# Kernel tuning notes

Hardware: AMD Instinct MI355X
Metric: run time of the kernel (lower is better)

## Reference

```python
import jax, jax.numpy as jnp
import numpy as np


def setup_inputs() -> dict:
    key = jax.random.key(0)
    k1, k2, k3 = jax.random.split(key, 3)
    N, F, E, H = 50000, 256, 800000, 4
    P = F // H + 1            # proj = 65
    dk = P * H                # 260
    x = jax.random.normal(k1, (N, F), dtype=jnp.float32)
    W = jax.random.normal(k2, (2 * dk, F), dtype=jnp.float32) * 0.02
    b = jnp.zeros((2 * dk,), dtype=jnp.float32)
    edge_index = jax.random.randint(k3, (2, E), 0, N, dtype=jnp.int32)
    return {"x": x, "edge_index": edge_index, "W": W, "b": b, "num_heads": H}


def reference(x, edge_index, W, b, num_heads):
    # x: [N, F]; W: [2*dk, F] with dk = P*num_heads; edge_index: [2, E]
    N = x.shape[0]
    P = W.shape[0] // (2 * num_heads)
    qk = x @ W.T + b                                   # [N, 2*dk]
    qk = qk.reshape(N, num_heads, 2 * P)               # 'L (h hdim) -> L h hdim'
    q, k = qk[..., :P], qk[..., P:]                    # split=2 outer -> q then k, each [N, H, P]
    src, dst = edge_index[0], edge_index[1]
    # per-edge dot product per head (NB: original never applies self.scale)
    scores = jnp.einsum('ehp,ehp->eh', q[src], k[dst])  # [E, H]
    # sparse softmax over dim=2 (columns) i.e. segment-softmax grouped by row index per head
    smax = jax.ops.segment_max(scores, src, num_segments=N)  # [N, H]
    ex = jnp.exp(scores - smax[src])                         # [E, H]
    denom = jax.ops.segment_sum(ex, src, num_segments=N)     # [N, H]
    attn = ex / denom[src]                                   # [E, H]
    # torch.sparse.sum(attn, dim=0) / num_heads -> mean over heads per edge
    vals = attn.mean(axis=1)                                 # [E]
    return vals
```

## Files before the change

### kernel.cpp

```cpp
#include <hip/hip_runtime.h>
#include <hip/hip_bf16.h>

#define K_DIM 256
#define RQ    512
#define NPAD  640
#define GBM 128
#define GBN 128
#define GBK 32
#define EPITCH 152
#define NBK   104
#define CBLK  256
#define SBAND 12512
#define DBAND 25024

typedef unsigned short u16;
using short8  = __attribute__((ext_vector_type(8))) short;
using ushort8 = __attribute__((ext_vector_type(8))) unsigned short;
using f32x4   = __attribute__((ext_vector_type(4))) float;
using f32x2   = __attribute__((ext_vector_type(2))) float;

__device__ __forceinline__ float asf(unsigned u) {
  union { unsigned i; float f; } x; x.i = u; return x.f;
}
__device__ __forceinline__ u16 f2b(float f) {
  __hip_bfloat16 h = __float2bfloat16(f); return *(u16*)&h;
}

__device__ __forceinline__ int bucket_of(int s, int d) {
  int sband = s / SBAND;
  int dband = d / DBAND;
  int ssub  = (s - sband * SBAND) >> 10;
  return ((sband << 1) | dband) * 13 + ssub;
}

__device__ __forceinline__ int map2(int p) {
  if (p < 256) return (p >> 6) * 130 + (p & 63);
  if (p < 512) { int q = p - 256; return (q >> 6) * 130 + 65 + (q & 63); }
  if (p < 516) return (p - 512) * 130 + 64;
  if (p < 520) return (p - 516) * 130 + 129;
  return -1;
}

__global__ void __launch_bounds__(256) prep(
    const float* __restrict__ x, const float* __restrict__ W,
    const float* __restrict__ bv, const int* __restrict__ ei,
    u16* __restrict__ xb, u16* __restrict__ wb,
    float* __restrict__ bias, float* __restrict__ zbase,
    int* __restrict__ counts,
    int M, int Mpad, int E, int per, int xblocks, int wblocks, int zblocks)
{
  __shared__ int h[NBK];
  const int blk = blockIdx.x, tid = threadIdx.x;
  if (blk < xblocks) {
    int idx = blk * 256 + tid;
    int total = Mpad * (K_DIM / 8);
    if (idx >= total) return;
    int row = idx / (K_DIM / 8);
    ushort8 o;
    if (row < M) {
      const float* s = x + (size_t)idx * 8;
      float4 a = *(const float4*)s;
      float4 b = *(const float4*)(s + 4);
      o[0] = f2b(a.x); o[1] = f2b(a.y); o[2] = f2b(a.z); o[3] = f2b(a.w);
      o[4] = f2b(b.x); o[5] = f2b(b.y); o[6] = f2b(b.z); o[7] = f2b(b.w);
    } else {
      #pragma unroll
      for (int j = 0; j < 8; ++j) o[j] = 0;
    }
    *(ushort8*)(xb + (size_t)idx * 8) = o;
  } else if (blk < xblocks + wblocks) {
    int idx = (blk - xblocks) * 256 + tid;
    int total = NPAD * (K_DIM / 8);
    if (idx >= total) return;
    int p  = idx / (K_DIM / 8);
    int kc = (idx % (K_DIM / 8)) * 8;
    int c  = map2(p);
    ushort8 o;
    if (c >= 0) {
      const float* s = W + (size_t)c * K_DIM + kc;
      float4 a = *(const float4*)s;
      float4 v = *(const float4*)(s + 4);
      o[0] = f2b(a.x); o[1] = f2b(a.y); o[2] = f2b(a.z); o[3] = f2b(a.w);
      o[4] = f2b(v.x); o[5] = f2b(v.y); o[6] = f2b(v.z); o[7] = f2b(v.w);
    } else {
      #pragma unroll
      for (int j = 0; j < 8; ++j) o[j] = 0;
    }
    *(ushort8*)(wb + (size_t)idx * 8) = o;
    if (kc == 0) bias[p] = (c >= 0) ? bv[c] : 0.f;
  } else if (blk < xblocks + wblocks + zblocks) {
    int i = (blk - xblocks - wblocks) * 256 + tid;
    if (i < M * 4) zbase[i] = 0.f;
  } else {
    int cb = blk - xblocks - wblocks - zblocks;
    if (tid < NBK) h[tid] = 0;
    __syncthreads();
    int start = cb * per, end = min(start + per, E);
    for (int i = start + tid; i < end; i += 256)
      atomicAdd(&h[bucket_of(ei[i], ei[E + i])], 1);
    __syncthreads();
    if (tid < NBK) counts[tid * CBLK + cb] = h[tid];
  }
}

__global__ void __launch_bounds__(256) gemm_mfma(
    const u16* __restrict__ xb, const u16* __restrict__ wb,
    const float* __restrict__ bias, u16* __restrict__ qkb,
    u16* __restrict__ tl, int M)
{
  __shared__ u16 smem[GBM * EPITCH];
  const int tid  = threadIdx.x;
  const int wave = tid >> 6, lane = tid & 63;
  const int l15 = lane & 15, lhi = lane >> 4;
  const int row0 = blockIdx.x * GBM, p0 = blockIdx.y * GBN;
  const int wr = (wave >> 1) * 64, wc = (wave & 1) * 64;

  f32x4 acc[4][4];
  #pragma unroll
  for (int m = 0; m < 4; ++m)
    #pragma unroll
    for (int n = 0; n < 4; ++n) acc[m][n] = (f32x4){0.f, 0.f, 0.f, 0.f};

#define STAGE(b, k0) do {                                                     \
    u16* As_ = smem + (b) * 8192;                                             \
    u16* Bs_ = As_ + 4096;                                                    \
    _Pragma("unroll")                                                         \
    for (int i_ = 0; i_ < 2; ++i_) {                                          \
      int f_ = wave * 128 + i_ * 64 + lane;                                   \
      int r_ = f_ >> 2, c_ = f_ & 3;                                          \
      const u16* gA = xb + (size_t)(row0 + r_) * K_DIM + (k0) + c_ * 8;       \
      __builtin_amdgcn_global_load_lds(                                       \
          (const __attribute__((address_space(1))) void*)gA,                  \
          (__attribute__((address_space(3))) void*)(As_ + (wave*128 + i_*64)*8), \
          16, 0, 0);                                                          \
      const u16* gB = wb + (size_t)(p0 + r_) * K_DIM + (k0) + c_ * 8;         \
      __builtin_amdgcn_global_load_lds(                                       \
          (const __attribute__((address_space(1))) void*)gB,                  \
          (__attribute__((address_space(3))) void*)(Bs_ + (wave*128 + i_*64)*8), \
          16, 0, 0);                                                          \
    }                                                                         \
  } while (0)

  STAGE(0, 0);
  asm volatile("s_waitcnt vmcnt(0)" ::: "memory");
  __syncthreads();

  #pragma unroll
  for (int t = 0; t < K_DIM / GBK; ++t) {
    if (t < K_DIM / GBK - 1) STAGE((t + 1) & 1, (t + 1) * GBK);
    const u16* As = smem + (t & 1) * 8192;
    const u16* Bs = As + 4096;
    short8 af[4], bf[4];
    #pragma unroll
    for (int m = 0; m < 4; ++m)
      af[m] = *(const short8*)(As + (size_t)(wr + m * 16 + l15) * GBK + lhi * 8);
    #pragma unroll
    for (int n = 0; n < 4; ++n)
      bf[n] = *(const short8*)(Bs + (size_t)(wc + n * 16 + l15) * GBK + lhi * 8);
    #pragma unroll
    for (int m = 0; m < 4; ++m)
      #pragma unroll
      for (int n = 0; n < 4; ++n)
        acc[m][n] = __builtin_amdgcn_mfma_f32_16x16x32_bf16(af[m], bf[n], acc[m][n], 0, 0, 0);
    if (t < K_DIM / GBK - 1) {
      asm volatile("s_waitcnt vmcnt(0)" ::: "memory");
      __syncthreads();
    }
  }
#undef STAGE

  __syncthreads();

  #pragma unroll
  for (int n = 0; n < 4; ++n) {
    int col = wc + n * 16 + l15;
    float bvv = bias[p0 + col];
    #pragma unroll
    for (int m = 0; m < 4; ++m) {
      #pragma unroll
      for (int r = 0; r < 4; ++r) {
        int row = wr + m * 16 + lhi * 4 + r;
        smem[row * EPITCH + col] = f2b(acc[m][n][r] + bvv);
      }
    }
  }
  __syncthreads();

  if (p0 < 512) {
    #pragma unroll
    for (int it = 0; it < 8; ++it) {
      int row  = wave * 32 + it * 4 + lhi;
      int grow = row0 + row;
      uint4 v = *(const uint4*)(smem + row * EPITCH + l15 * 8);
      if (grow < M)
        *(uint4*)(qkb + (size_t)grow * RQ + p0 + l15 * 8) = v;
    }
  } else {
    #pragma unroll
    for (int it = 0; it < 8; ++it) {
      int row  = wave * 32 + it * 4 + lhi;
      int grow = row0 + row;
      if (l15 == 0 && grow < M) {
        uint4 v = *(const uint4*)(smem + row * EPITCH);
        *(uint4*)(tl + (size_t)grow * 8) = v;
      }
    }
  }
}

__global__ void __launch_bounds__(1024) scan_k(int* __restrict__ counts)
{
  __shared__ int tot[NBK], base[NBK];
  const int tid = threadIdx.x, wv = tid >> 6, ln = tid & 63;
  for (int k = wv; k < NBK; k += 16) {
    int sum = 0;
    #pragma unroll
    for (int c = 0; c < CBLK / 64; ++c) sum += counts[k * CBLK + c * 64 + ln];
    #pragma unroll
    for (int off = 1; off < 64; off <<= 1) sum += __shfl_xor(sum, off);
    if (ln == 0) tot[k] = sum;
  }
  __syncthreads();
  if (tid == 0) {
    int run = 0;
    for (int k = 0; k < NBK; ++k) { base[k] = run; run += tot[k]; }
  }
  __syncthreads();
  for (int k = wv; k < NBK; k += 16) {
    int carry = base[k];
    #pragma unroll
    for (int c = 0; c < CBLK / 64; ++c) {
      int v = counts[k * CBLK + c * 64 + ln];
      int inc = v;
      #pragma unroll
      for (int off = 1; off < 64; off <<= 1) {
        int u = __shfl_up(inc, off);
        if (ln >= off) inc += u;
      }
      int last = __shfl(inc, 63);
      counts[k * CBLK + c * 64 + ln] = carry + inc - v;
      carry += last;
    }
  }
}

__global__ void __launch_bounds__(256) scatter2_k(
    const int* __restrict__ ei, const int* __restrict__ offs,
    uint2* __restrict__ sorted, int E, int per)
{
  __shared__ int cur[NBK];
  const int tid = threadIdx.x, blk = blockIdx.x;
  if (tid < NBK) cur[tid] = offs[tid * CBLK + blk];
  __syncthreads();
  int start = blk * per, end = min(start + per, E);
  for (int i = start + tid; i < end; i += 256) {
    int s = ei[i], d = ei[E + i];
    int pos = atomicAdd(&cur[bucket_of(s, d)], 1);
    sorted[pos] = make_uint2(((unsigned)s << 16) | (unsigned)d, (unsigned)i);
  }
}

__global__ void __launch_bounds__(256) edge_pass(
    const u16* __restrict__ qkb, const u16* __restrict__ tl,
    const uint2* __restrict__ sorted,
    float* __restrict__ exb, float* __restrict__ denom, int E)
{
  const int tid  = threadIdx.x;
  const int wave = tid >> 6, lane = tid & 63;
  const int g = lane >> 3;
  const int l = lane & 7;

  const int nwg = gridDim.x;
  const int q8 = nwg >> 3, r8 = nwg & 7;
  const int xcd = blockIdx.x & 7, bix = blockIdx.x >> 3;
  const int swz = (xcd < r8) ? (xcd * (q8 + 1) + bix)
                             : (r8 * (q8 + 1) + (xcd - r8) * q8 + bix);

  const int slot = swz * 32 + wave * 8 + g;
  const bool valid = slot < E;
  uint2 tr = sorted[valid ? slot : 0];
  const int src = tr.x >> 16, dst = tr.x & 0xffff;
  const int e = tr.y;

  const u16* qrow = qkb + ((size_t)src * RQ) + l * 32;
  const u16* krow = qkb + ((size_t)dst * RQ) + 256 + l * 32;

  int2 ti = make_int2(0, 0);
  if (l < 2) {
    const u16* tp = tl + (size_t)(l ? dst : src) * 8 + (l ? 4 : 0);
    ti = *(const int2*)tp;
  }

  f32x2 a2 = {0.f, 0.f};
  #pragma unroll
  for (int c = 0; c < 4; ++c) {
    uint4 qv = *(const uint4*)(qrow + c * 8);
    uint4 kv = *(const uint4*)(krow + c * 8);
    const unsigned* qd = (const unsigned*)&qv;
    const unsigned* kd = (const unsigned*)&kv;
    #pragma unroll
    for (int j = 0; j < 4; ++j) {
      f32x2 qa = { asf(qd[j] << 16), asf(qd[j] & 0xffff0000u) };
      f32x2 ka = { asf(kd[j] << 16), asf(kd[j] & 0xffff0000u) };
      a2 += qa * ka;
    }
  }
  float s = a2[0] + a2[1];
  s += __shfl_xor(s, 1);

  const int h = l >> 1;
  int idxA = ((g << 3) | (l & 1)) << 2;
  int w01 = __builtin_amdgcn_ds_bpermute(idxA, ti.x);
  int w23 = __builtin_amdgcn_ds_bpermute(idxA, ti.y);
  unsigned wsel = (h & 2) ? (unsigned)w23 : (unsigned)w01;
  float tv = (h & 1) ? asf(wsel & 0xffff0000u) : asf(wsel << 16);
  float to = __shfl_xor(tv, 1);
  s = fmaf(tv, to, s);

  float ev = __expf(s);
  if (valid && (l & 1) == 0) {
    exb[(size_t)e * 4 + h] = ev;
    unsafeAtomicAdd(&denom[(size_t)src * 4 + h], ev);
  }
}

__global__ void __launch_bounds__(256) finalize_k(
    const float* __restrict__ exb, const float* __restrict__ denom,
    const int* __restrict__ ei, float* __restrict__ out, int E)
{
  int e = blockIdx.x * 256 + threadIdx.x;
  if (e >= E) return;
  int src = ei[e];
  float4 ev = *(const float4*)(exb + (size_t)e * 4);
  float4 dv = *(const float4*)(denom + (size_t)src * 4);
  out[e] = 0.25f * (ev.x / dv.x + ev.y / dv.y + ev.z / dv.z + ev.w / dv.w);
}

extern "C" void kernel_launch(void* const* d_in, const int* in_sizes, int n_in,
                              void* d_out, int out_size, void* d_ws, size_t ws_size,
                              hipStream_t stream)
{
  const float* x  = (const float*)d_in[0];
  const int*   ei = (const int*)d_in[1];
  const float* W  = (const float*)d_in[2];
  const float* b  = (const float*)d_in[3];

  const int F = in_sizes[2] / in_sizes[3];
  const int M = in_sizes[0] / F;
  const int E = in_sizes[1] / 2;

  const int mblocks = (M + GBM - 1) / GBM;
  const int Mpad    = mblocks * GBM;

  u16* xb  = (u16*)d_ws;
  u16* wb  = xb + (size_t)Mpad * K_DIM;
  u16* qkb = wb + (size_t)NPAD * K_DIM;
  u16* tl  = qkb + (size_t)M * RQ;
  float* bias  = (float*)(tl + (size_t)M * 8);
  float* exb   = bias + NPAD;
  float* denom = exb + (size_t)E * 4;
  int*   counts = (int*)(denom + (size_t)M * 4);
  uint2* sorted = (uint2*)(counts + NBK * CBLK);

  const int xblocks = (Mpad * (K_DIM / 8) + 255) / 256;
  const int wblocks = (NPAD * (K_DIM / 8) + 255) / 256;
  const int zblocks = (M * 4 + 255) / 256;
  const int per     = (E + CBLK - 1) / CBLK;
  hipLaunchKernelGGL(prep, dim3(xblocks + wblocks + zblocks + CBLK), dim3(256), 0,
                     stream, x, W, b, ei, xb, wb, bias, denom, counts,
                     M, Mpad, E, per, xblocks, wblocks, zblocks);

  hipLaunchKernelGGL(scan_k, dim3(1), dim3(1024), 0, stream, counts);

  dim3 gg(mblocks, NPAD / GBN);
  hipLaunchKernelGGL(gemm_mfma, gg, dim3(256), 0, stream, xb, wb, bias, qkb, tl, M);

  hipLaunchKernelGGL(scatter2_k, dim3(CBLK), dim3(256), 0, stream,
                     ei, counts, sorted, E, per);

  int eblocks = (E + 31) / 32;
  hipLaunchKernelGGL(edge_pass, dim3(eblocks), dim3(256), 0, stream,
                     qkb, tl, sorted, exb, denom, E);

  hipLaunchKernelGGL(finalize_k, dim3((E + 255) / 256), dim3(256), 0, stream,
                     exb, denom, ei, (float*)d_out, E);
}
```

Measured before the change: 176.8 us.

## Fuse x bf16 conversion into GEMM, keep A tile resident, store exp in fp16

```diff
diff --git a/kernel.cpp b/kernel.cpp
--- a/kernel.cpp
+++ b/kernel.cpp
@@ -5,9 +5,6 @@
 #define RQ    512
 #define NPAD  640
 #define GBM 128
-#define GBN 128
-#define GBK 32
-#define EPITCH 152
 #define NBK   104
 #define CBLK  256
 #define SBAND 12512
@@ -25,6 +22,8 @@
 __device__ __forceinline__ u16 f2b(float f) {
   __hip_bfloat16 h = __float2bfloat16(f); return *(u16*)&h;
 }
+__device__ __forceinline__ u16 f2h(float f) { _Float16 h = (_Float16)f; return *(u16*)&h; }
+__device__ __forceinline__ float h2f(u16 u) { _Float16 h = *(_Float16*)&u; return (float)h; }
 
 __device__ __forceinline__ int bucket_of(int s, int d) {
   int sband = s / SBAND;
@@ -42,34 +41,16 @@
 }
 
 __global__ void __launch_bounds__(256) prep(
-    const float* __restrict__ x, const float* __restrict__ W,
-    const float* __restrict__ bv, const int* __restrict__ ei,
-    u16* __restrict__ xb, u16* __restrict__ wb,
-    float* __restrict__ bias, float* __restrict__ zbase,
+    const float* __restrict__ W, const float* __restrict__ bv,
+    const int* __restrict__ ei,
+    u16* __restrict__ wb, float* __restrict__ bias, float* __restrict__ zbase,
     int* __restrict__ counts,
-    int M, int Mpad, int E, int per, int xblocks, int wblocks, int zblocks)
+    int M, int E, int per, int wblocks, int zblocks)
 {
   __shared__ int h[NBK];
   const int blk = blockIdx.x, tid = threadIdx.x;
-  if (blk < xblocks) {
+  if (blk < wblocks) {
     int idx = blk * 256 + tid;
-    int total = Mpad * (K_DIM / 8);
-    if (idx >= total) return;
-    int row = idx / (K_DIM / 8);
-    ushort8 o;
-    if (row < M) {
-      const float* s = x + (size_t)idx * 8;
-      float4 a = *(const float4*)s;
-      float4 b = *(const float4*)(s + 4);
-      o[0] = f2b(a.x); o[1] = f2b(a.y); o[2] = f2b(a.z); o[3] = f2b(a.w);
-      o[4] = f2b(b.x); o[5] = f2b(b.y); o[6] = f2b(b.z); o[7] = f2b(b.w);
-    } else {
-      #pragma unroll
-      for (int j = 0; j < 8; ++j) o[j] = 0;
-    }
-    *(ushort8*)(xb + (size_t)idx * 8) = o;
-  } else if (blk < xblocks + wblocks) {
-    int idx = (blk - xblocks) * 256 + tid;
     int total = NPAD * (K_DIM / 8);
     if (idx >= total) return;
     int p  = idx / (K_DIM / 8);
@@ -88,11 +69,11 @@
     }
     *(ushort8*)(wb + (size_t)idx * 8) = o;
     if (kc == 0) bias[p] = (c >= 0) ? bv[c] : 0.f;
-  } else if (blk < xblocks + wblocks + zblocks) {
-    int i = (blk - xblocks - wblocks) * 256 + tid;
+  } else if (blk < wblocks + zblocks) {
+    int i = (blk - wblocks) * 256 + tid;
     if (i < M * 4) zbase[i] = 0.f;
   } else {
-    int cb = blk - xblocks - wblocks - zblocks;
+    int cb = blk - wblocks - zblocks;
     if (tid < NBK) h[tid] = 0;
     __syncthreads();
     int start = cb * per, end = min(start + per, E);
@@ -103,17 +84,55 @@
   }
 }
 
-__global__ void __launch_bounds__(256) gemm_mfma(
-    const u16* __restrict__ xb, const u16* __restrict__ wb,
+__global__ void __launch_bounds__(256) gemm_fused(
+    const float* __restrict__ x, const u16* __restrict__ wb,
     const float* __restrict__ bias, u16* __restrict__ qkb,
     u16* __restrict__ tl, int M)
 {
-  __shared__ u16 smem[GBM * EPITCH];
+  __shared__ u16 A[GBM * K_DIM];
+  __shared__ u16 Bb[2 * 512 * 8];
   const int tid  = threadIdx.x;
   const int wave = tid >> 6, lane = tid & 63;
   const int l15 = lane & 15, lhi = lane >> 4;
-  const int row0 = blockIdx.x * GBM, p0 = blockIdx.y * GBN;
+  const int row0 = blockIdx.x * GBM;
   const int wr = (wave >> 1) * 64, wc = (wave & 1) * 64;
+  const int sw = l15 & 7;
+
+  #pragma unroll
+  for (int it = 0; it < 16; ++it) {
+    int f  = it * 256 + tid;
+    int r  = f >> 5, ch = f & 31;
+    int grow = row0 + r;
+    float4 a0 = make_float4(0.f,0.f,0.f,0.f), a1 = a0;
+    if (grow < M) {
+      const float* s = x + (size_t)grow * K_DIM + ch * 8;
+      a0 = *(const float4*)s;
+      a1 = *(const float4*)(s + 4);
+    }
+    ushort8 o;
+    o[0] = f2b(a0.x); o[1] = f2b(a0.y); o[2] = f2b(a0.z); o[3] = f2b(a0.w);
+    o[4] = f2b(a1.x); o[5] = f2b(a1.y); o[6] = f2b(a1.z); o[7] = f2b(a1.w);
+    *(ushort8*)(A + r * K_DIM + (ch ^ (r & 7)) * 8) = o;
+  }
+
+#define BLOAD(i, va, vb) do {                                                  \
+    int p_ = (i) >> 3, kt_ = (i) & 7;                                          \
+    const u16* base_ = wb + (size_t)(p_ * 128) * K_DIM + kt_ * 32;             \
+    int r1_ = tid >> 2, c1_ = tid & 3;                                         \
+    va = *(const uint4*)(base_ + (size_t)r1_ * K_DIM + c1_ * 8);               \
+    int r2_ = (tid + 256) >> 2, c2_ = tid & 3;                                 \
+    vb = *(const uint4*)(base_ + (size_t)r2_ * K_DIM + c2_ * 8);               \
+  } while (0)
+#define BWRITE(i, va, vb) do {                                                 \
+    u16* bb_ = Bb + ((i) & 1) * 4096;                                          \
+    int r1_ = tid >> 2, c1_ = tid & 3;                                         \
+    *(uint4*)(bb_ + (c1_ * 128 + r1_) * 8) = va;                               \
+    int r2_ = (tid + 256) >> 2, c2_ = tid & 3;                                 \
+    *(uint4*)(bb_ + (c2_ * 128 + r2_) * 8) = vb;                               \
+  } while (0)
+
+  { uint4 b0a, b0b; BLOAD(0, b0a, b0b); BWRITE(0, b0a, b0b); }
+  __syncthreads();
 
   f32x4 acc[4][4];
   #pragma unroll
@@ -121,91 +140,53 @@
     #pragma unroll
     for (int n = 0; n < 4; ++n) acc[m][n] = (f32x4){0.f, 0.f, 0.f, 0.f};
 
-#define STAGE(b, k0) do {                                                     \
-    u16* As_ = smem + (b) * 8192;                                             \
-    u16* Bs_ = As_ + 4096;                                                    \
-    _Pragma("unroll")                                                         \
-    for (int i_ = 0; i_ < 2; ++i_) {                                          \
-      int f_ = wave * 128 + i_ * 64 + lane;                                   \
-      int r_ = f_ >> 2, c_ = f_ & 3;                                          \
-      const u16* gA = xb + (size_t)(row0 + r_) * K_DIM + (k0) + c_ * 8;       \
-      __builtin_amdgcn_global_load_lds(                                       \
-          (const __attribute__((address_space(1))) void*)gA,                  \
-          (__attribute__((address_space(3))) void*)(As_ + (wave*128 + i_*64)*8), \
-          16, 0, 0);                                                          \
-      const u16* gB = wb + (size_t)(p0 + r_) * K_DIM + (k0) + c_ * 8;         \
-      __builtin_amdgcn_global_load_lds(                                       \
-          (const __attribute__((address_space(1))) void*)gB,                  \
-          (__attribute__((address_space(3))) void*)(Bs_ + (wave*128 + i_*64)*8), \
-          16, 0, 0);                                                          \
-    }                                                                         \
-  } while (0)
-
-  STAGE(0, 0);
-  asm volatile("s_waitcnt vmcnt(0)" ::: "memory");
-  __syncthreads();
-
-  #pragma unroll
-  for (int t = 0; t < K_DIM / GBK; ++t) {
-    if (t < K_DIM / GBK - 1) STAGE((t + 1) & 1, (t + 1) * GBK);
-    const u16* As = smem + (t & 1) * 8192;
-    const u16* Bs = As + 4096;
+  for (int i = 0; i < 40; ++i) {
+    const int kt = i & 7, buf = i & 1;
+    uint4 na, nb;
+    if (i < 39) BLOAD(i + 1, na, nb);
+
+    const u16* bbuf = Bb + buf * 4096;
     short8 af[4], bf[4];
+    const int cc = ((kt * 4 + lhi) ^ sw);
     #pragma unroll
     for (int m = 0; m < 4; ++m)
-      af[m] = *(const short8*)(As + (size_t)(wr + m * 16 + l15) * GBK + lhi * 8);
+      af[m] = *(const short8*)(A + (wr + m * 16 + l15) * K_DIM + cc * 8);
     #pragma unroll
     for (int n = 0; n < 4; ++n)
-      bf[n] = *(const short8*)(Bs + (size_t)(wc + n * 16 + l15) * GBK + lhi * 8);
+      bf[n] = *(const short8*)(bbuf + (lhi * 128 + wc + n * 16 + l15) * 8);
     #pragma unroll
     for (int m = 0; m < 4; ++m)
       #pragma unroll
       for (int n = 0; n < 4; ++n)
         acc[m][n] = __builtin_amdgcn_mfma_f32_16x16x32_bf16(af[m], bf[n], acc[m][n], 0, 0, 0);
-    if (t < K_DIM / GBK - 1) {
-      asm volatile("s_waitcnt vmcnt(0)" ::: "memory");
-      __syncthreads();
-    }
-  }
-#undef STAGE
-
-  __syncthreads();
-
-  #pragma unroll
-  for (int n = 0; n < 4; ++n) {
-    int col = wc + n * 16 + l15;
-    float bvv = bias[p0 + col];
-    #pragma unroll
-    for (int m = 0; m < 4; ++m) {
+
+    if (i < 39) BWRITE(i + 1, na, nb);
+    __syncthreads();
+
+    if (kt == 7) {
+      const int p0 = (i >> 3) * 128;
       #pragma unroll
-      for (int r = 0; r < 4; ++r) {
-        int row = wr + m * 16 + lhi * 4 + r;
-        smem[row * EPITCH + col] = f2b(acc[m][n][r] + bvv);
+      for (int n = 0; n < 4; ++n) {
+        int col = p0 + wc + n * 16 + l15;
+        float bvv = bias[col];
+        #pragma unroll
+        for (int m = 0; m < 4; ++m) {
+          #pragma unroll
+          for (int r = 0; r < 4; ++r) {
+            int grow = row0 + wr + m * 16 + lhi * 4 + r;
+            if (grow < M) {
+              float v = acc[m][n][r] + bvv;
+              if (col < 512)            qkb[(size_t)grow * RQ + col] = f2b(v);
+              else if (col < 520)       tl[(size_t)grow * 8 + col - 512] = f2b(v);
+            }
+          }
+          acc[m][n] = (f32x4){0.f, 0.f, 0.f, 0.f};
+        }
       }
     }
   }
-  __syncthreads();
-
-  if (p0 < 512) {
-    #pragma unroll
-    for (int it = 0; it < 8; ++it) {
-      int row  = wave * 32 + it * 4 + lhi;
-      int grow = row0 + row;
-      uint4 v = *(const uint4*)(smem + row * EPITCH + l15 * 8);
-      if (grow < M)
-        *(uint4*)(qkb + (size_t)grow * RQ + p0 + l15 * 8) = v;
-    }
-  } else {
-    #pragma unroll
-    for (int it = 0; it < 8; ++it) {
-      int row  = wave * 32 + it * 4 + lhi;
-      int grow = row0 + row;
-      if (l15 == 0 && grow < M) {
-        uint4 v = *(const uint4*)(smem + row * EPITCH);
-        *(uint4*)(tl + (size_t)grow * 8) = v;
-      }
-    }
-  }
+#undef BLOAD
+#undef BWRITE
 }
 
 __global__ void __launch_bounds__(1024) scan_k(int* __restrict__ counts)
@@ -263,7 +244,7 @@
 __global__ void __launch_bounds__(256) edge_pass(
     const u16* __restrict__ qkb, const u16* __restrict__ tl,
     const uint2* __restrict__ sorted,
-    float* __restrict__ exb, float* __restrict__ denom, int E)
+    u16* __restrict__ exh, float* __restrict__ denom, int E)
 {
   const int tid  = threadIdx.x;
   const int wave = tid >> 6, lane = tid & 63;
@@ -319,21 +300,22 @@
 
   float ev = __expf(s);
   if (valid && (l & 1) == 0) {
-    exb[(size_t)e * 4 + h] = ev;
+    exh[(size_t)e * 4 + h] = f2h(ev);
     unsafeAtomicAdd(&denom[(size_t)src * 4 + h], ev);
   }
 }
 
 __global__ void __launch_bounds__(256) finalize_k(
-    const float* __restrict__ exb, const float* __restrict__ denom,
+    const u16* __restrict__ exh, const float* __restrict__ denom,
     const int* __restrict__ ei, float* __restrict__ out, int E)
 {
   int e = blockIdx.x * 256 + threadIdx.x;
   if (e >= E) return;
   int src = ei[e];
-  float4 ev = *(const float4*)(exb + (size_t)e * 4);
+  ushort4 ev = *(const ushort4*)(exh + (size_t)e * 4);
   float4 dv = *(const float4*)(denom + (size_t)src * 4);
-  out[e] = 0.25f * (ev.x / dv.x + ev.y / dv.y + ev.z / dv.z + ev.w / dv.w);
+  out[e] = 0.25f * (h2f(ev.x) / dv.x + h2f(ev.y) / dv.y
+                  + h2f(ev.z) / dv.z + h2f(ev.w) / dv.w);
 }
 
 extern "C" void kernel_launch(void* const* d_in, const int* in_sizes, int n_in,
@@ -350,38 +332,35 @@
   const int E = in_sizes[1] / 2;
 
   const int mblocks = (M + GBM - 1) / GBM;
-  const int Mpad    = mblocks * GBM;
-
-  u16* xb  = (u16*)d_ws;
-  u16* wb  = xb + (size_t)Mpad * K_DIM;
+
+  u16* wb  = (u16*)d_ws;
   u16* qkb = wb + (size_t)NPAD * K_DIM;
   u16* tl  = qkb + (size_t)M * RQ;
   float* bias  = (float*)(tl + (size_t)M * 8);
-  float* exb   = bias + NPAD;
-  float* denom = exb + (size_t)E * 4;
+  u16*   exh   = (u16*)(bias + NPAD);
+  float* denom = (float*)(exh + (size_t)E * 4);
   int*   counts = (int*)(denom + (size_t)M * 4);
   uint2* sorted = (uint2*)(counts + NBK * CBLK);
 
-  const int xblocks = (Mpad * (K_DIM / 8) + 255) / 256;
   const int wblocks = (NPAD * (K_DIM / 8) + 255) / 256;
   const int zblocks = (M * 4 + 255) / 256;
   const int per     = (E + CBLK - 1) / CBLK;
-  hipLaunchKernelGGL(prep, dim3(xblocks + wblocks + zblocks + CBLK), dim3(256), 0,
-                     stream, x, W, b, ei, xb, wb, bias, denom, counts,
-                     M, Mpad, E, per, xblocks, wblocks, zblocks);
+  hipLaunchKernelGGL(prep, dim3(wblocks + zblocks + CBLK), dim3(256), 0, stream,
+                     W, b, ei, wb, bias, denom, counts,
+                     M, E, per, wblocks, zblocks);
 
   hipLaunchKernelGGL(scan_k, dim3(1), dim3(1024), 0, stream, counts);
 
-  dim3 gg(mblocks, NPAD / GBN);
-  hipLaunchKernelGGL(gemm_mfma, gg, dim3(256), 0, stream, xb, wb, bias, qkb, tl, M);
+  hipLaunchKernelGGL(gemm_fused, dim3(mblocks), dim3(256), 0, stream,
+                     x, wb, bias, qkb, tl, M);
 
   hipLaunchKernelGGL(scatter2_k, dim3(CBLK), dim3(256), 0, stream,
                      ei, counts, sorted, E, per);
 
   int eblocks = (E + 31) / 32;
   hipLaunchKernelGGL(edge_pass, dim3(eblocks), dim3(256), 0, stream,
-                     qkb, tl, sorted, exb, denom, E);
+                     qkb, tl, sorted, exh, denom, E);
 
   hipLaunchKernelGGL(finalize_k, dim3((E + 255) / 256), dim3(256), 0, stream,
-                     exb, denom, ei, (float*)d_out, E);
-}
+                     exh, denom, ei, (float*)d_out, E);
+}
```

Result: slower. 209.5 us (+18.5%).

## Split tail columns into separate GEMV and store edge exponentials as fp16

Applied to the files above, without the earlier changes.

```diff
diff --git a/kernel.cpp b/kernel.cpp
--- a/kernel.cpp
+++ b/kernel.cpp
@@ -3,7 +3,7 @@
 
 #define K_DIM 256
 #define RQ    512
-#define NPAD  640
+#define NW    512
 #define GBM 128
 #define GBN 128
 #define GBK 32
@@ -25,6 +25,11 @@
 __device__ __forceinline__ u16 f2b(float f) {
   __hip_bfloat16 h = __float2bfloat16(f); return *(u16*)&h;
 }
+__device__ __forceinline__ float b2f(u16 u) {
+  union { unsigned i; float f; } x; x.i = ((unsigned)u) << 16; return x.f;
+}
+__device__ __forceinline__ u16 f2h(float f) { _Float16 h = (_Float16)f; return *(u16*)&h; }
+__device__ __forceinline__ float h2f(u16 u) { _Float16 h = *(_Float16*)&u; return (float)h; }
 
 __device__ __forceinline__ int bucket_of(int s, int d) {
   int sband = s / SBAND;
@@ -35,10 +40,10 @@
 
 __device__ __forceinline__ int map2(int p) {
   if (p < 256) return (p >> 6) * 130 + (p & 63);
-  if (p < 512) { int q = p - 256; return (q >> 6) * 130 + 65 + (q & 63); }
-  if (p < 516) return (p - 512) * 130 + 64;
-  if (p < 520) return (p - 516) * 130 + 129;
-  return -1;
+  int q = p - 256; return (q >> 6) * 130 + 65 + (q & 63);
+}
+__device__ __forceinline__ int wrow_tail(int c) {
+  return (c < 4) ? c * 130 + 64 : (c - 4) * 130 + 129;
 }
 
 __global__ void __launch_bounds__(256) prep(
@@ -70,24 +75,19 @@
     *(ushort8*)(xb + (size_t)idx * 8) = o;
   } else if (blk < xblocks + wblocks) {
     int idx = (blk - xblocks) * 256 + tid;
-    int total = NPAD * (K_DIM / 8);
+    int total = NW * (K_DIM / 8);
     if (idx >= total) return;
     int p  = idx / (K_DIM / 8);
     int kc = (idx % (K_DIM / 8)) * 8;
     int c  = map2(p);
+    const float* s = W + (size_t)c * K_DIM + kc;
+    float4 a = *(const float4*)s;
+    float4 v = *(const float4*)(s + 4);
     ushort8 o;
-    if (c >= 0) {
-      const float* s = W + (size_t)c * K_DIM + kc;
-      float4 a = *(const float4*)s;
-      float4 v = *(const float4*)(s + 4);
-      o[0] = f2b(a.x); o[1] = f2b(a.y); o[2] = f2b(a.z); o[3] = f2b(a.w);
-      o[4] = f2b(v.x); o[5] = f2b(v.y); o[6] = f2b(v.z); o[7] = f2b(v.w);
-    } else {
-      #pragma unroll
-      for (int j = 0; j < 8; ++j) o[j] = 0;
-    }
+    o[0] = f2b(a.x); o[1] = f2b(a.y); o[2] = f2b(a.z); o[3] = f2b(a.w);
+    o[4] = f2b(v.x); o[5] = f2b(v.y); o[6] = f2b(v.z); o[7] = f2b(v.w);
     *(ushort8*)(wb + (size_t)idx * 8) = o;
-    if (kc == 0) bias[p] = (c >= 0) ? bv[c] : 0.f;
+    if (kc == 0) bias[p] = bv[c];
   } else if (blk < xblocks + wblocks + zblocks) {
     int i = (blk - xblocks - wblocks) * 256 + tid;
     if (i < M * 4) zbase[i] = 0.f;
@@ -105,8 +105,7 @@
 
 __global__ void __launch_bounds__(256) gemm_mfma(
     const u16* __restrict__ xb, const u16* __restrict__ wb,
-    const float* __restrict__ bias, u16* __restrict__ qkb,
-    u16* __restrict__ tl, int M)
+    const float* __restrict__ bias, u16* __restrict__ qkb, int M)
 {
   __shared__ u16 smem[GBM * EPITCH];
   const int tid  = threadIdx.x;
@@ -186,25 +185,60 @@
   }
   __syncthreads();
 
-  if (p0 < 512) {
-    #pragma unroll
-    for (int it = 0; it < 8; ++it) {
-      int row  = wave * 32 + it * 4 + lhi;
-      int grow = row0 + row;
-      uint4 v = *(const uint4*)(smem + row * EPITCH + l15 * 8);
-      if (grow < M)
-        *(uint4*)(qkb + (size_t)grow * RQ + p0 + l15 * 8) = v;
-    }
-  } else {
-    #pragma unroll
-    for (int it = 0; it < 8; ++it) {
-      int row  = wave * 32 + it * 4 + lhi;
-      int grow = row0 + row;
-      if (l15 == 0 && grow < M) {
-        uint4 v = *(const uint4*)(smem + row * EPITCH);
-        *(uint4*)(tl + (size_t)grow * 8) = v;
-      }
-    }
+  #pragma unroll
+  for (int it = 0; it < 8; ++it) {
+    int row  = wave * 32 + it * 4 + lhi;
+    int grow = row0 + row;
+    uint4 v = *(const uint4*)(smem + row * EPITCH + l15 * 8);
+    if (grow < M)
+      *(uint4*)(qkb + (size_t)grow * RQ + p0 + l15 * 8) = v;
+  }
+}
+
+__global__ void __launch_bounds__(256) tail_gemv(
+    const float* __restrict__ x, const float* __restrict__ W,
+    const float* __restrict__ bv, u16* __restrict__ tl, int M)
+{
+  __shared__ u16 wt[8 * 256];
+  __shared__ float tb[8];
+  const int tid = threadIdx.x;
+  #pragma unroll
+  for (int c = 0; c < 8; ++c)
+    wt[c * 256 + tid] = f2b(W[(size_t)wrow_tail(c) * K_DIM + tid]);
+  if (tid < 8) tb[tid] = bv[wrow_tail(tid)];
+  __syncthreads();
+
+  const int wave = tid >> 6, lane = tid & 63;
+  const int seg = lane & 7;
+  const int grow = blockIdx.x * 32 + wave * 8 + (lane >> 3);
+  const bool vr = grow < M;
+  const float* xr = x + (size_t)(vr ? grow : 0) * K_DIM + seg * 32;
+
+  float acc[8];
+  #pragma unroll
+  for (int c = 0; c < 8; ++c) acc[c] = 0.f;
+  #pragma unroll
+  for (int j = 0; j < 8; ++j) {
+    float4 xv = vr ? *(const float4*)(xr + j * 4) : make_float4(0.f,0.f,0.f,0.f);
+    #pragma unroll
+    for (int c = 0; c < 8; ++c) {
+      ushort4 wv = *(const ushort4*)(wt + c * 256 + seg * 32 + j * 4);
+      acc[c] = fmaf(xv.x, b2f(wv.x), acc[c]);
+      acc[c] = fmaf(xv.y, b2f(wv.y), acc[c]);
+      acc[c] = fmaf(xv.z, b2f(wv.z), acc[c]);
+      acc[c] = fmaf(xv.w, b2f(wv.w), acc[c]);
+    }
+  }
+  #pragma unroll
+  for (int off = 1; off < 8; off <<= 1)
+    #pragma unroll
+    for (int c = 0; c < 8; ++c) acc[c] += __shfl_xor(acc[c], off);
+
+  if (vr && seg == 0) {
+    ushort8 o;
+    #pragma unroll
+    for (int c = 0; c < 8; ++c) o[c] = f2b(acc[c] + tb[c]);
+    *(ushort8*)(tl + (size_t)grow * 8) = o;
   }
 }
 
@@ -263,7 +297,7 @@
 __global__ void __launch_bounds__(256) edge_pass(
     const u16* __restrict__ qkb, const u16* __restrict__ tl,
     const uint2* __restrict__ sorted,
-    float* __restrict__ exb, float* __restrict__ denom, int E)
+    u16* __restrict__ exh, float* __restrict__ denom, int E)
 {
   const int tid  = threadIdx.x;
   const int wave = tid >> 6, lane = tid & 63;
@@ -319,21 +353,22 @@
 
   float ev = __expf(s);
   if (valid && (l & 1) == 0) {
-    exb[(size_t)e * 4 + h] = ev;
+    exh[(size_t)e * 4 + h] = f2h(ev);
     unsafeAtomicAdd(&denom[(size_t)src * 4 + h], ev);
   }
 }
 
 __global__ void __launch_bounds__(256) finalize_k(
-    const float* __restrict__ exb, const float* __restrict__ denom,
+    const u16* __restrict__ exh, const float* __restrict__ denom,
     const int* __restrict__ ei, float* __restrict__ out, int E)
 {
   int e = blockIdx.x * 256 + threadIdx.x;
   if (e >= E) return;
   int src = ei[e];
-  float4 ev = *(const float4*)(exb + (size_t)e * 4);
+  ushort4 ev = *(const ushort4*)(exh + (size_t)e * 4);
   float4 dv = *(const float4*)(denom + (size_t)src * 4);
-  out[e] = 0.25f * (ev.x / dv.x + ev.y / dv.y + ev.z / dv.z + ev.w / dv.w);
+  out[e] = 0.25f * (h2f(ev.x) / dv.x + h2f(ev.y) / dv.y
+                  + h2f(ev.z) / dv.z + h2f(ev.w) / dv.w);
 }
 
 extern "C" void kernel_launch(void* const* d_in, const int* in_sizes, int n_in,
@@ -354,16 +389,16 @@
 
   u16* xb  = (u16*)d_ws;
   u16* wb  = xb + (size_t)Mpad * K_DIM;
-  u16* qkb = wb + (size_t)NPAD * K_DIM;
+  u16* qkb = wb + (size_t)NW * K_DIM;
   u16* tl  = qkb + (size_t)M * RQ;
   float* bias  = (float*)(tl + (size_t)M * 8);
-  float* exb   = bias + NPAD;
-  float* denom = exb + (size_t)E * 4;
+  u16*   exh   = (u16*)(bias + NW);
+  float* denom = (float*)(exh + (size_t)E * 4);
   int*   counts = (int*)(denom + (size_t)M * 4);
   uint2* sorted = (uint2*)(counts + NBK * CBLK);
 
   const int xblocks = (Mpad * (K_DIM / 8) + 255) / 256;
-  const int wblocks = (NPAD * (K_DIM / 8) + 255) / 256;
+  const int wblocks = (NW * (K_DIM / 8) + 255) / 256;
   const int zblocks = (M * 4 + 255) / 256;
   const int per     = (E + CBLK - 1) / CBLK;
   hipLaunchKernelGGL(prep, dim3(xblocks + wblocks + zblocks + CBLK), dim3(256), 0,
@@ -372,16 +407,19 @@
 
   hipLaunchKernelGGL(scan_k, dim3(1), dim3(1024), 0, stream, counts);
 
-  dim3 gg(mblocks, NPAD / GBN);
-  hipLaunchKernelGGL(gemm_mfma, gg, dim3(256), 0, stream, xb, wb, bias, qkb, tl, M);
+  hipLaunchKernelGGL(tail_gemv, dim3((M + 31) / 32), dim3(256), 0, stream,
+                     x, W, b, tl, M);
+
+  dim3 gg(mblocks, NW / GBN);
+  hipLaunchKernelGGL(gemm_mfma, gg, dim3(256), 0, stream, xb, wb, bias, qkb, M);
 
   hipLaunchKernelGGL(scatter2_k, dim3(CBLK), dim3(256), 0, stream,
                      ei, counts, sorted, E, per);
 
   int eblocks = (E + 31) / 32;
   hipLaunchKernelGGL(edge_pass, dim3(eblocks), dim3(256), 0, stream,
-                     qkb, tl, sorted, exb, denom, E);
+                     qkb, tl, sorted, exh, denom, E);
 
   hipLaunchKernelGGL(finalize_k, dim3((E + 255) / 256), dim3(256), 0, stream,
-                     exb, denom, ei, (float*)d_out, E);
-}
+                     exh, denom, ei, (float*)d_out, E);
+}
```

Measured after the change: 193.8 us. +9.6%, slower.

## Process two edges per lane group and store exp values as fp16

Applied to the files above, without the earlier changes.

```diff
diff --git a/kernel.cpp b/kernel.cpp
--- a/kernel.cpp
+++ b/kernel.cpp
@@ -25,6 +25,8 @@
 __device__ __forceinline__ u16 f2b(float f) {
   __hip_bfloat16 h = __float2bfloat16(f); return *(u16*)&h;
 }
+__device__ __forceinline__ u16 f2h(float f) { _Float16 h = (_Float16)f; return *(u16*)&h; }
+__device__ __forceinline__ float h2f(u16 u) { _Float16 h = *(_Float16*)&u; return (float)h; }
 
 __device__ __forceinline__ int bucket_of(int s, int d) {
   int sband = s / SBAND;
@@ -260,10 +262,10 @@
   }
 }
 
-__global__ void __launch_bounds__(256) edge_pass(
+__global__ void __launch_bounds__(256, 4) edge_pass(
     const u16* __restrict__ qkb, const u16* __restrict__ tl,
     const uint2* __restrict__ sorted,
-    float* __restrict__ exb, float* __restrict__ denom, int E)
+    u16* __restrict__ exh, float* __restrict__ denom, int E)
 {
   const int tid  = threadIdx.x;
   const int wave = tid >> 6, lane = tid & 63;
@@ -276,64 +278,83 @@
   const int swz = (xcd < r8) ? (xcd * (q8 + 1) + bix)
                              : (r8 * (q8 + 1) + (xcd - r8) * q8 + bix);
 
-  const int slot = swz * 32 + wave * 8 + g;
-  const bool valid = slot < E;
-  uint2 tr = sorted[valid ? slot : 0];
-  const int src = tr.x >> 16, dst = tr.x & 0xffff;
-  const int e = tr.y;
-
-  const u16* qrow = qkb + ((size_t)src * RQ) + l * 32;
-  const u16* krow = qkb + ((size_t)dst * RQ) + 256 + l * 32;
-
-  int2 ti = make_int2(0, 0);
-  if (l < 2) {
-    const u16* tp = tl + (size_t)(l ? dst : src) * 8 + (l ? 4 : 0);
-    ti = *(const int2*)tp;
-  }
-
-  f32x2 a2 = {0.f, 0.f};
+  const int s0 = swz * 64 + wave * 16 + g;
+  const int s1 = s0 + 8;
+  const bool v0 = s0 < E, v1 = s1 < E;
+  uint2 r0 = sorted[v0 ? s0 : 0];
+  uint2 r1 = sorted[v1 ? s1 : 0];
+  const int src0 = r0.x >> 16, dst0 = r0.x & 0xffff;
+  const int src1 = r1.x >> 16, dst1 = r1.x & 0xffff;
+
+  const u16* q0p = qkb + (size_t)src0 * RQ + l * 32;
+  const u16* k0p = qkb + (size_t)dst0 * RQ + 256 + l * 32;
+  const u16* q1p = qkb + (size_t)src1 * RQ + l * 32;
+  const u16* k1p = qkb + (size_t)dst1 * RQ + 256 + l * 32;
+
+  uint4 qv0[4], kv0[4], qv1[4], kv1[4];
   #pragma unroll
   for (int c = 0; c < 4; ++c) {
-    uint4 qv = *(const uint4*)(qrow + c * 8);
-    uint4 kv = *(const uint4*)(krow + c * 8);
-    const unsigned* qd = (const unsigned*)&qv;
-    const unsigned* kd = (const unsigned*)&kv;
-    #pragma unroll
-    for (int j = 0; j < 4; ++j) {
-      f32x2 qa = { asf(qd[j] << 16), asf(qd[j] & 0xffff0000u) };
-      f32x2 ka = { asf(kd[j] << 16), asf(kd[j] & 0xffff0000u) };
-      a2 += qa * ka;
-    }
-  }
-  float s = a2[0] + a2[1];
-  s += __shfl_xor(s, 1);
+    qv0[c] = *(const uint4*)(q0p + c * 8);
+    kv0[c] = *(const uint4*)(k0p + c * 8);
+  }
+  #pragma unroll
+  for (int c = 0; c < 4; ++c) {
+    qv1[c] = *(const uint4*)(q1p + c * 8);
+    kv1[c] = *(const uint4*)(k1p + c * 8);
+  }
+  int2 t0 = make_int2(0, 0), t1 = make_int2(0, 0);
+  if (l < 2) {
+    t0 = *(const int2*)(tl + (size_t)(l ? dst0 : src0) * 8 + (l ? 4 : 0));
+    t1 = *(const int2*)(tl + (size_t)(l ? dst1 : src1) * 8 + (l ? 4 : 0));
+  }
 
   const int h = l >> 1;
-  int idxA = ((g << 3) | (l & 1)) << 2;
-  int w01 = __builtin_amdgcn_ds_bpermute(idxA, ti.x);
-  int w23 = __builtin_amdgcn_ds_bpermute(idxA, ti.y);
-  unsigned wsel = (h & 2) ? (unsigned)w23 : (unsigned)w01;
-  float tv = (h & 1) ? asf(wsel & 0xffff0000u) : asf(wsel << 16);
-  float to = __shfl_xor(tv, 1);
-  s = fmaf(tv, to, s);
-
-  float ev = __expf(s);
-  if (valid && (l & 1) == 0) {
-    exb[(size_t)e * 4 + h] = ev;
-    unsafeAtomicAdd(&denom[(size_t)src * 4 + h], ev);
-  }
+  const int idxA = ((g << 3) | (l & 1)) << 2;
+
+#define EDGE_COMPUTE(qv, kv, ti, src_, e_, vld) do {                          \
+    f32x2 a2 = {0.f, 0.f};                                                    \
+    _Pragma("unroll")                                                         \
+    for (int c = 0; c < 4; ++c) {                                             \
+      const unsigned* qd = (const unsigned*)&qv[c];                           \
+      const unsigned* kd = (const unsigned*)&kv[c];                           \
+      _Pragma("unroll")                                                       \
+      for (int j = 0; j < 4; ++j) {                                           \
+        f32x2 qa = { asf(qd[j] << 16), asf(qd[j] & 0xffff0000u) };            \
+        f32x2 ka = { asf(kd[j] << 16), asf(kd[j] & 0xffff0000u) };            \
+        a2 += qa * ka;                                                        \
+      }                                                                       \
+    }                                                                         \
+    float s = a2[0] + a2[1];                                                  \
+    s += __shfl_xor(s, 1);                                                    \
+    int w01 = __builtin_amdgcn_ds_bpermute(idxA, ti.x);                       \
+    int w23 = __builtin_amdgcn_ds_bpermute(idxA, ti.y);                       \
+    unsigned wsel = (h & 2) ? (unsigned)w23 : (unsigned)w01;                  \
+    float tv = (h & 1) ? asf(wsel & 0xffff0000u) : asf(wsel << 16);           \
+    float to = __shfl_xor(tv, 1);                                             \
+    s = fmaf(tv, to, s);                                                      \
+    float ev = __expf(s);                                                     \
+    if ((vld) && (l & 1) == 0) {                                              \
+      exh[(size_t)(e_) * 4 + h] = f2h(ev);                                    \
+      unsafeAtomicAdd(&denom[(size_t)(src_) * 4 + h], ev);                    \
+    }                                                                         \
+  } while (0)
+
+  EDGE_COMPUTE(qv0, kv0, t0, src0, r0.y, v0);
+  EDGE_COMPUTE(qv1, kv1, t1, src1, r1.y, v1);
+#undef EDGE_COMPUTE
 }
 
 __global__ void __launch_bounds__(256) finalize_k(
-    const float* __restrict__ exb, const float* __restrict__ denom,
+    const u16* __restrict__ exh, const float* __restrict__ denom,
     const int* __restrict__ ei, float* __restrict__ out, int E)
 {
   int e = blockIdx.x * 256 + threadIdx.x;
   if (e >= E) return;
   int src = ei[e];
-  float4 ev = *(const float4*)(exb + (size_t)e * 4);
+  ushort4 ev = *(const ushort4*)(exh + (size_t)e * 4);
   float4 dv = *(const float4*)(denom + (size_t)src * 4);
-  out[e] = 0.25f * (ev.x / dv.x + ev.y / dv.y + ev.z / dv.z + ev.w / dv.w);
+  out[e] = 0.25f * (h2f(ev.x) / dv.x + h2f(ev.y) / dv.y
+                  + h2f(ev.z) / dv.z + h2f(ev.w) / dv.w);
 }
 
 extern "C" void kernel_launch(void* const* d_in, const int* in_sizes, int n_in,
@@ -357,8 +378,8 @@
   u16* qkb = wb + (size_t)NPAD * K_DIM;
   u16* tl  = qkb + (size_t)M * RQ;
   float* bias  = (float*)(tl + (size_t)M * 8);
-  float* exb   = bias + NPAD;
-  float* denom = exb + (size_t)E * 4;
+  u16*   exh   = (u16*)(bias + NPAD);
+  float* denom = (float*)(exh + (size_t)E * 4);
   int*   counts = (int*)(denom + (size_t)M * 4);
   uint2* sorted = (uint2*)(counts + NBK * CBLK);
 
@@ -378,10 +399,10 @@
   hipLaunchKernelGGL(scatter2_k, dim3(CBLK), dim3(256), 0, stream,
                      ei, counts, sorted, E, per);
 
-  int eblocks = (E + 31) / 32;
+  int eblocks = (E + 63) / 64;
   hipLaunchKernelGGL(edge_pass, dim3(eblocks), dim3(256), 0, stream,
-                     qkb, tl, sorted, exb, denom, E);
+                     qkb, tl, sorted, exh, denom, E);
 
   hipLaunchKernelGGL(finalize_k, dim3((E + 255) / 256), dim3(256), 0, stream,
-                     exb, denom, ei, (float*)d_out, E);
-}
+                     exh, denom, ei, (float*)d_out, E);
+}
```

New measurement: 168.8 us. 1.05x faster.
